# Kernel optimization log

Hardware: AMD Instinct MI355X
Metric: run time of the kernel (lower is better)

## Reference

```python
import jax, jax.numpy as jnp
from jax import lax
import numpy as np


def setup_inputs() -> dict:
    key = jax.random.key(0)
    k1, k2, k3 = jax.random.split(key, 3)
    B, H, W, C = 8, 128, 128, 128
    F, KS = 128, 3
    x = jax.random.normal(k1, (B, H, W, C), dtype=jnp.float32)
    style = jax.random.normal(k2, (B, C), dtype=jnp.float32)
    kernel = jax.random.normal(k3, (KS, KS, C, F), dtype=jnp.float32) * 0.05
    return {"x": x, "style": style, "kernel": kernel}


def reference(x, style, kernel):
    """StyleGAN2 modulated+demodulated conv via grouped conv (groups=batch).
    x: (B,H,W,C) NHWC, style: (B,C), kernel: (kh,kw,C,F)."""
    B, H, W, C = x.shape
    kh, kw, Cin, F = kernel.shape
    # Modulate: per-sample scale of input channels -> (B, kh, kw, C, F)
    w = kernel[None] * (style[:, None, None, :, None] + 1.0)
    # Demodulate: normalize each output filter over (kh, kw, Cin)
    w = w / jnp.sqrt(jnp.sum(jnp.square(w), axis=(1, 2, 3), keepdims=True) + 1e-8)
    # Grouped conv trick: fold batch into channels, groups = B
    xg = jnp.transpose(x, (0, 3, 1, 2)).reshape(1, B * C, H, W)   # (1, B*C, H, W)
    wg = jnp.transpose(w, (1, 2, 3, 0, 4)).reshape(kh, kw, Cin, B * F)  # HWIO
    y = lax.conv_general_dilated(
        xg, wg, window_strides=(1, 1), padding="SAME",
        dimension_numbers=("NCHW", "HWIO", "NCHW"),
        feature_group_count=B,
    )  # (1, B*F, H, W)
    y = y.reshape(B, F, H, W)
    return jnp.transpose(y, (0, 2, 3, 1))  # NHWC
```

## Files before the change

### kernel.cpp

```cpp
#include <hip/hip_runtime.h>

typedef __attribute__((ext_vector_type(8))) short short8;
typedef __attribute__((ext_vector_type(8))) unsigned short ushort8;
typedef __attribute__((ext_vector_type(4))) float f32x4;

static __device__ __forceinline__ unsigned short f2bf(float f) {
    union { float f; unsigned int u; } a; a.f = f;
    unsigned int u = a.u;
    return (unsigned short)((u + 0x7fffu + ((u >> 16) & 1u)) >> 16);
}

__global__ void prep_sumsq(const float* __restrict__ kern,
                           const float* __restrict__ style,
                           float* __restrict__ partial) {
    const int rs = blockIdx.x;
    const int b  = blockIdx.y;
    const int t  = threadIdx.x;
    __shared__ float sty[128];
    __shared__ float red[256];
    if (t < 128) sty[t] = style[b * 128 + t] + 1.0f;
    __syncthreads();
    const int f = t & 127, half = t >> 7;
    const float* kp = kern + (size_t)rs * 16384 + f;
    float s = 0.0f;
    #pragma unroll 8
    for (int c = half * 64; c < half * 64 + 64; ++c) {
        float w = kp[(size_t)c * 128] * sty[c];
        s += w * w;
    }
    red[t] = s;
    __syncthreads();
    if (t < 128) partial[((size_t)b * 9 + rs) * 128 + t] = red[t] + red[t + 128];
}

__global__ void prep_wt(const float* __restrict__ kern,
                        const float* __restrict__ style,
                        const float* __restrict__ partial,
                        unsigned short* __restrict__ wt) {
    const int rs = blockIdx.x, b = blockIdx.y;
    const int t  = threadIdx.x;
    __shared__ float sty[128], dm[128];
    __shared__ float ts[32][132];
    if (t < 128) {
        sty[t] = style[b * 128 + t] + 1.0f;
    } else {
        const int f = t - 128;
        float s = 0.0f;
        #pragma unroll
        for (int r = 0; r < 9; ++r) s += partial[((size_t)b * 9 + r) * 128 + f];
        dm[f] = rsqrtf(s + 1e-8f);
    }
    __syncthreads();
    const float* kp = kern + (size_t)rs * 16384;
    unsigned short* wp = wt + ((size_t)b * 9 + rs) * 16384;
    for (int c0 = 0; c0 < 128; c0 += 32) {
        {
            const int fi = (t & 31) * 4;
            const int ci = t >> 5;
            #pragma unroll
            for (int k = 0; k < 4; ++k) {
                const float4 v = *(const float4*)(kp + (size_t)(c0 + ci + 8 * k) * 128 + fi);
                ts[ci + 8 * k][fi + 0] = v.x;
                ts[ci + 8 * k][fi + 1] = v.y;
                ts[ci + 8 * k][fi + 2] = v.z;
                ts[ci + 8 * k][fi + 3] = v.w;
            }
        }
        __syncthreads();
        {
            const int cb = (t & 7) * 4;
            const int f2 = t >> 3;
            #pragma unroll
            for (int k = 0; k < 4; ++k) {
                const int f = f2 + 32 * k;
                ushort4 o;
                o.x = f2bf(ts[cb + 0][f] * sty[c0 + cb + 0] * dm[f]);
                o.y = f2bf(ts[cb + 1][f] * sty[c0 + cb + 1] * dm[f]);
                o.z = f2bf(ts[cb + 2][f] * sty[c0 + cb + 2] * dm[f]);
                o.w = f2bf(ts[cb + 3][f] * sty[c0 + cb + 3] * dm[f]);
                *(ushort4*)(wp + (size_t)f * 128 + c0 + cb) = o;
            }
        }
        __syncthreads();
    }
}

#define PROW 16640
#define PPLANE 2163200
__global__ void cvt_x(const float* __restrict__ x, unsigned short* __restrict__ xbf) {
    const int id = blockIdx.x * 256 + threadIdx.x;
    if (id >= 8 * 130 * 130 * 16) return;
    const int cg = id & 15;
    const int p  = id >> 4;
    const int wp = p % 130;
    const int q  = p / 130;
    const int hp = q % 130;
    const int b  = q / 130;
    ushort8 v = {0, 0, 0, 0, 0, 0, 0, 0};
    if (hp >= 1 && hp <= 128 && wp >= 1 && wp <= 128) {
        const float4* src = (const float4*)(x + (((size_t)b * 128 + (hp - 1)) * 128 + (wp - 1)) * 128 + cg * 8);
        float4 f0 = src[0];
        float4 f1 = src[1];
        v[0] = f2bf(f0.x); v[1] = f2bf(f0.y); v[2] = f2bf(f0.z); v[3] = f2bf(f0.w);
        v[4] = f2bf(f1.x); v[5] = f2bf(f1.y); v[6] = f2bf(f1.z); v[7] = f2bf(f1.w);
    }
    *(ushort8*)(xbf + (size_t)p * 128 + cg * 8) = v;
}

__global__ __launch_bounds__(512) void mdconv2(const unsigned short* __restrict__ xbf,
                                               const unsigned short* __restrict__ wt,
                                               float* __restrict__ out) {
    const int lin = blockIdx.x;
    const int fh  = lin & 1;
    const int spg = (lin >> 1) & 31;
    const int b   = lin >> 6;
    const int tid = threadIdx.x;

    __shared__ unsigned short wtl[9 * 64 * 136];

    {
        for (int idx = tid; idx < 576 * 16; idx += 512) {
            const int row = idx >> 4;
            const int c8  = idx & 15;
            const int rs  = row >> 6;
            const int f   = row & 63;
            const ushort8 v = *(const ushort8*)(wt + (((size_t)b * 9 + rs) * 128 + fh * 64 + f) * 128 + c8 * 8);
            *(ushort8*)(wtl + row * 136 + c8 * 8) = v;
        }
    }
    __syncthreads();

    const int lane = tid & 63;
    const int wv   = tid >> 6;
    const int fl   = lane & 15;
    const int quad = lane >> 4;
    const int kq   = quad * 8;

    const int hrow  = spg * 4 + (wv >> 1);
    const int wbase = (wv & 1) * 64;

    f32x4 acc[4][4];
    #pragma unroll
    for (int mt = 0; mt < 4; ++mt)
        #pragma unroll
        for (int ft = 0; ft < 4; ++ft)
            acc[mt][ft] = (f32x4){0.f, 0.f, 0.f, 0.f};

    const unsigned short* xb = xbf + (size_t)b * PPLANE;

    #pragma unroll
    for (int rs = 0; rs < 9; ++rs) {
        const int r = rs / 3, s = rs % 3;
        const unsigned short* arow = xb + ((size_t)(hrow + r) * 130 + wbase + s) * 128 + fl * 128 + kq;
        const unsigned short* brow = wtl + (size_t)rs * (64 * 136) + fl * 136 + kq;
        #pragma unroll
        for (int kc = 0; kc < 4; ++kc) {
            short8 a[4];
            #pragma unroll
            for (int mt = 0; mt < 4; ++mt)
                a[mt] = *(const short8*)(arow + mt * 16 * 128 + kc * 32);
            short8 bf[4];
            #pragma unroll
            for (int ft = 0; ft < 4; ++ft)
                bf[ft] = *(const short8*)(brow + ft * 16 * 136 + kc * 32);
            #pragma unroll
            for (int mt = 0; mt < 4; ++mt)
                #pragma unroll
                for (int ft = 0; ft < 4; ++ft)
                    acc[mt][ft] =
                        __builtin_amdgcn_mfma_f32_16x16x32_bf16(a[mt], bf[ft], acc[mt][ft], 0, 0, 0);
        }
    }

    float* ob = out + ((size_t)(b * 128 + hrow) * 128) * 128;
    #pragma unroll
    for (int mt = 0; mt < 4; ++mt) {
        #pragma unroll
        for (int ft = 0; ft < 4; ++ft) {
            const int f = fh * 64 + ft * 16 + fl;
            #pragma unroll
            for (int reg = 0; reg < 4; ++reg) {
                const int w = wbase + mt * 16 + quad * 4 + reg;
                ob[(size_t)w * 128 + f] = acc[mt][ft][reg];
            }
        }
    }
}

__global__ void mdconv_fb(const float* __restrict__ x,
                          const unsigned short* __restrict__ wt,
                          float* __restrict__ out) {
    const int lin = blockIdx.x;
    const int b   = lin & 7;
    const int sp  = lin >> 3;
    const int h0  = (sp >> 3) * 8;
    const int w0  = (sp & 7) * 16;
    const int tid = threadIdx.x;
    __shared__ unsigned short xs[180 * 138];
    {
        const float* xb = x + (size_t)b * (128 * 128 * 128);
        for (int id = tid; id < 180 * 16; id += 256) {
            int p  = id >> 4;
            int cg = id & 15;
            int pr = p / 18;
            int pc = p - pr * 18;
            int hh = h0 - 1 + pr;
            int ww = w0 - 1 + pc;
            ushort8 v = {0, 0, 0, 0, 0, 0, 0, 0};
            if ((unsigned)hh < 128u && (unsigned)ww < 128u) {
                const float4* src = (const float4*)(xb + ((size_t)(hh * 128 + ww) * 128 + cg * 8));
                float4 f0 = src[0];
                float4 f1 = src[1];
                v[0] = f2bf(f0.x); v[1] = f2bf(f0.y); v[2] = f2bf(f0.z); v[3] = f2bf(f0.w);
                v[4] = f2bf(f1.x); v[5] = f2bf(f1.y); v[6] = f2bf(f1.z); v[7] = f2bf(f1.w);
            }
            *(ushort8*)(xs + p * 138 + cg * 8) = v;
        }
    }
    __syncthreads();
    const int lane = tid & 63;
    const int wave = tid >> 6;
    const int fl   = lane & 15;
    const int quad = lane >> 4;
    const int kq   = quad * 8;
    f32x4 acc[8][2];
    #pragma unroll
    for (int mt = 0; mt < 8; ++mt)
        #pragma unroll
        for (int j = 0; j < 2; ++j)
            acc[mt][j] = (f32x4){0.f, 0.f, 0.f, 0.f};
    const unsigned short* wtb = wt + (size_t)b * (9 * 128 * 128) + (size_t)wave * 4096 + fl * 128 + kq;
    #pragma unroll
    for (int rs = 0; rs < 9; ++rs) {
        const int r = rs / 3, s = rs % 3;
        #pragma unroll
        for (int kc = 0; kc < 4; ++kc) {
            const int k0 = kc * 32 + kq;
            short8 a[8];
            #pragma unroll
            for (int mt = 0; mt < 8; ++mt)
                a[mt] = *(const short8*)(xs + ((mt + r) * 18 + fl + s) * 138 + k0);
            #pragma unroll
            for (int j = 0; j < 2; ++j) {
                short8 bf = *(const short8*)(wtb + rs * 16384 + j * 2048 + kc * 32);
                #pragma unroll
                for (int mt = 0; mt < 8; ++mt)
                    acc[mt][j] = __builtin_amdgcn_mfma_f32_16x16x32_bf16(a[mt], bf, acc[mt][j], 0, 0, 0);
            }
        }
    }
    float* ob = out + ((size_t)(b * 128 + h0) * 128 + w0) * 128;
    #pragma unroll
    for (int mt = 0; mt < 8; ++mt)
        #pragma unroll
        for (int j = 0; j < 2; ++j) {
            const int f = (wave * 2 + j) * 16 + fl;
            #pragma unroll
            for (int reg = 0; reg < 4; ++reg)
                ob[((size_t)(mt * 128 + quad * 4 + reg)) * 128 + f] = acc[mt][j][reg];
        }
}

extern "C" void kernel_launch(void* const* d_in, const int* in_sizes, int n_in,
                              void* d_out, int out_size, void* d_ws, size_t ws_size,
                              hipStream_t stream) {
    const float* x     = (const float*)d_in[0];
    const float* style = (const float*)d_in[1];
    const float* kern  = (const float*)d_in[2];
    float* out = (float*)d_out;

    const size_t XBF_BYTES = (size_t)8 * 130 * 130 * 128 * 2;
    const size_t WT_BYTES  = (size_t)8 * 9 * 128 * 128 * 2;
    const size_t NEED      = XBF_BYTES + WT_BYTES + 36864;

    if (ws_size >= NEED) {
        unsigned short* xbf = (unsigned short*)d_ws;
        unsigned short* wt  = (unsigned short*)((char*)d_ws + XBF_BYTES);
        float* partial      = (float*)((char*)d_ws + XBF_BYTES + WT_BYTES);
        prep_sumsq<<<dim3(9, 8), dim3(256), 0, stream>>>(kern, style, partial);
        prep_wt<<<dim3(9, 8), dim3(256), 0, stream>>>(kern, style, partial, wt);
        cvt_x<<<dim3((8 * 130 * 130 * 16 + 255) / 256), dim3(256), 0, stream>>>(x, xbf);
        mdconv2<<<dim3(512), dim3(512), 0, stream>>>(xbf, wt, out);
    } else {
        unsigned short* wt = (unsigned short*)d_ws;
        float* partial     = (float*)((char*)d_ws + WT_BYTES);
        prep_sumsq<<<dim3(9, 8), dim3(256), 0, stream>>>(kern, style, partial);
        prep_wt<<<dim3(9, 8), dim3(256), 0, stream>>>(kern, style, partial, wt);
        mdconv_fb<<<dim3(1024), dim3(256), 0, stream>>>(x, wt, out);
    }
}
```

Before: 204.1 us.

## Double-buffer A and B tiles in LDS via direct global-to-LDS loads

Replaces the main conv kernel with one where each 256-thread block computes a full output row (128 pixels x 128 filters) for one batch. The 36 reduction stages (9 taps x 4 channel chunks) stream both input and weight tiles into a double-buffered LDS region using global_load_lds, overlapping the next stage's loads with the current MFMAs. Previously, activations were read straight from global into registers and weights were staged once per block. The goal is to hide global latency and cut redundant register-path loads. The cost is a barrier per stage and unpadded LDS rows that may cause bank conflicts.

```diff
diff --git a/kernel.cpp b/kernel.cpp
--- a/kernel.cpp
+++ b/kernel.cpp
@@ -8,6 +8,12 @@
     union { float f; unsigned int u; } a; a.f = f;
     unsigned int u = a.u;
     return (unsigned short)((u + 0x7fffu + ((u >> 16) & 1u)) >> 16);
+}
+
+static __device__ __forceinline__ void gll16(const unsigned short* g, unsigned short* l) {
+    __builtin_amdgcn_global_load_lds(
+        (const __attribute__((address_space(1))) unsigned int*)g,
+        (__attribute__((address_space(3))) unsigned int*)l, 16, 0, 0);
 }
 
 __global__ void prep_sumsq(const float* __restrict__ kern,
@@ -107,37 +113,29 @@
     *(ushort8*)(xbf + (size_t)p * 128 + cg * 8) = v;
 }
 
-__global__ __launch_bounds__(512) void mdconv2(const unsigned short* __restrict__ xbf,
-                                               const unsigned short* __restrict__ wt,
-                                               float* __restrict__ out) {
+__global__ __launch_bounds__(256, 4) void mdconv6(const unsigned short* __restrict__ xbf,
+                                                  const unsigned short* __restrict__ wt,
+                                                  float* __restrict__ out) {
     const int lin = blockIdx.x;
-    const int fh  = lin & 1;
-    const int spg = (lin >> 1) & 31;
-    const int b   = lin >> 6;
+    const int b   = lin & 7;
+    const int h   = lin >> 3;
     const int tid = threadIdx.x;
 
-    __shared__ unsigned short wtl[9 * 64 * 136];
-
-    {
-        for (int idx = tid; idx < 576 * 16; idx += 512) {
-            const int row = idx >> 4;
-            const int c8  = idx & 15;
-            const int rs  = row >> 6;
-            const int f   = row & 63;
-            const ushort8 v = *(const ushort8*)(wt + (((size_t)b * 9 + rs) * 128 + fh * 64 + f) * 128 + c8 * 8);
-            *(ushort8*)(wtl + row * 136 + c8 * 8) = v;
-        }
-    }
-    __syncthreads();
+    __shared__ unsigned short lsh[2 * 8192];
+
+    const unsigned short* xb  = xbf + (size_t)b * PPLANE;
+    const unsigned short* wtb = wt + (size_t)b * 9 * 16384;
+
+    const int a0off = (tid >> 2) * 128 + (tid & 3) * 8;
 
     const int lane = tid & 63;
     const int wv   = tid >> 6;
     const int fl   = lane & 15;
     const int quad = lane >> 4;
-    const int kq   = quad * 8;
-
-    const int hrow  = spg * 4 + (wv >> 1);
-    const int wbase = (wv & 1) * 64;
+    const int wrb  = (wv >> 1) * 64;
+    const int fcb  = (wv & 1) * 64;
+    const int ab_rd = (wrb + fl) * 32 + quad * 8;
+    const int bb_rd = 4096 + (fcb + fl) * 32 + quad * 8;
 
     f32x4 acc[4][4];
     #pragma unroll
@@ -146,43 +144,50 @@
         for (int ft = 0; ft < 4; ++ft)
             acc[mt][ft] = (f32x4){0.f, 0.f, 0.f, 0.f};
 
-    const unsigned short* xb = xbf + (size_t)b * PPLANE;
-
-    #pragma unroll
-    for (int rs = 0; rs < 9; ++rs) {
-        const int r = rs / 3, s = rs % 3;
-        const unsigned short* arow = xb + ((size_t)(hrow + r) * 130 + wbase + s) * 128 + fl * 128 + kq;
-        const unsigned short* brow = wtl + (size_t)rs * (64 * 136) + fl * 136 + kq;
-        #pragma unroll
-        for (int kc = 0; kc < 4; ++kc) {
-            short8 a[4];
-            #pragma unroll
-            for (int mt = 0; mt < 4; ++mt)
-                a[mt] = *(const short8*)(arow + mt * 16 * 128 + kc * 32);
-            short8 bf[4];
+#define STAGE(st, nxt) {                                                          \
+    const int rs_ = (st) >> 2, kc_ = (st) & 3;                                    \
+    const int r_ = rs_ / 3, s_ = rs_ % 3;                                         \
+    const unsigned short* ga = xb + ((size_t)(h + r_) * 130 + s_) * 128 + kc_ * 32; \
+    const unsigned short* gb = wtb + rs_ * 16384 + kc_ * 32;                      \
+    unsigned short* la = lsh + (nxt) * 8192;                                      \
+    gll16(ga + a0off,        la + tid * 8);                                       \
+    gll16(ga + a0off + 8192, la + 2048 + tid * 8);                                \
+    gll16(gb + a0off,        la + 4096 + tid * 8);                                \
+    gll16(gb + a0off + 8192, la + 6144 + tid * 8);                                \
+}
+
+    STAGE(0, 0);
+    __syncthreads();
+
+    #pragma unroll
+    for (int st = 0; st < 36; ++st) {
+        const int cur = st & 1;
+        if (st < 35) STAGE(st + 1, cur ^ 1);
+        const int ce = cur * 8192;
+        short8 bv[4];
+        #pragma unroll
+        for (int ft = 0; ft < 4; ++ft)
+            bv[ft] = *(const short8*)(lsh + ce + bb_rd + ft * 512);
+        #pragma unroll
+        for (int mt = 0; mt < 4; ++mt) {
+            const short8 av = *(const short8*)(lsh + ce + ab_rd + mt * 512);
             #pragma unroll
             for (int ft = 0; ft < 4; ++ft)
-                bf[ft] = *(const short8*)(brow + ft * 16 * 136 + kc * 32);
-            #pragma unroll
-            for (int mt = 0; mt < 4; ++mt)
-                #pragma unroll
-                for (int ft = 0; ft < 4; ++ft)
-                    acc[mt][ft] =
-                        __builtin_amdgcn_mfma_f32_16x16x32_bf16(a[mt], bf[ft], acc[mt][ft], 0, 0, 0);
-        }
-    }
-
-    float* ob = out + ((size_t)(b * 128 + hrow) * 128) * 128;
+                acc[mt][ft] = __builtin_amdgcn_mfma_f32_16x16x32_bf16(av, bv[ft], acc[mt][ft], 0, 0, 0);
+        }
+        __syncthreads();
+    }
+#undef STAGE
+
+    float* ob = out + ((size_t)(b * 128 + h) * 128) * 128;
     #pragma unroll
     for (int mt = 0; mt < 4; ++mt) {
         #pragma unroll
-        for (int ft = 0; ft < 4; ++ft) {
-            const int f = fh * 64 + ft * 16 + fl;
-            #pragma unroll
-            for (int reg = 0; reg < 4; ++reg) {
-                const int w = wbase + mt * 16 + quad * 4 + reg;
-                ob[(size_t)w * 128 + f] = acc[mt][ft][reg];
-            }
+        for (int reg = 0; reg < 4; ++reg) {
+            const int w = wrb + mt * 16 + quad * 4 + reg;
+            #pragma unroll
+            for (int ft = 0; ft < 4; ++ft)
+                ob[(size_t)w * 128 + fcb + ft * 16 + fl] = acc[mt][ft][reg];
         }
     }
 }
@@ -280,7 +285,7 @@
         prep_sumsq<<<dim3(9, 8), dim3(256), 0, stream>>>(kern, style, partial);
         prep_wt<<<dim3(9, 8), dim3(256), 0, stream>>>(kern, style, partial, wt);
         cvt_x<<<dim3((8 * 130 * 130 * 16 + 255) / 256), dim3(256), 0, stream>>>(x, xbf);
-        mdconv2<<<dim3(512), dim3(512), 0, stream>>>(xbf, wt, out);
+        mdconv6<<<dim3(1024), dim3(256), 0, stream>>>(xbf, wt, out);
     } else {
         unsigned short* wt = (unsigned short*)d_ws;
         float* partial     = (float*)((char*)d_ws + WT_BYTES);
```

Result: faster. 165.6 us (-18.9%).
